# Optimization experiments

Hardware: AMD Instinct MI355X
Metric: run time of the kernel (lower is better)

Reference implementation:

```python
import jax, jax.numpy as jnp
import numpy as np

B, C, S, F = 128, 5, 512, 3
U = 256          # encoder units
RU = 2 * U       # decoder units / bidirectional encoder width


def _lstm_cell(x_t, h, c, Wk, Wr, b):
    # Keras LSTM gate order: i, f, g(cell), o
    z = x_t @ Wk + h @ Wr + b
    i, f, g, o = jnp.split(z, 4, axis=-1)
    c_new = jax.nn.sigmoid(f) * c + jax.nn.sigmoid(i) * jnp.tanh(g)
    h_new = jax.nn.sigmoid(o) * jnp.tanh(c_new)
    return h_new, c_new


def _masked_lstm(xs, mask, Wk, Wr, b, units):
    # xs: [B,S,D], mask: [B,S] bool. Keras semantics: masked steps carry
    # previous state and previous output (== previous h for LSTM).
    Bn = xs.shape[0]

    def step(carry, inp):
        h, c = carry
        x_t, m_t = inp
        h_n, c_n = _lstm_cell(x_t, h, c, Wk, Wr, b)
        m = m_t[:, None]
        h2 = jnp.where(m, h_n, h)
        c2 = jnp.where(m, c_n, c)
        return (h2, c2), h2

    init = (jnp.zeros((Bn, units), xs.dtype), jnp.zeros((Bn, units), xs.dtype))
    _, outs = jax.lax.scan(step, init, (jnp.swapaxes(xs, 0, 1), mask.T))
    return jnp.swapaxes(outs, 0, 1)  # [B,S,units]


def setup_inputs() -> dict:
    key = jax.random.key(0)
    k = jax.random.split(key, 10)
    s = 0.05
    rn = lambda kk, sh: jax.random.normal(kk, sh, jnp.float32) * s
    return {
        "x": jax.random.normal(k[0], (B, C, S, F), jnp.float32),
        "Wf_k": rn(k[1], (C, 4 * U)), "Wf_r": rn(k[2], (U, 4 * U)), "bf": jnp.zeros((4 * U,), jnp.float32),
        "Wb_k": rn(k[3], (C, 4 * U)), "Wb_r": rn(k[4], (U, 4 * U)), "bb": jnp.zeros((4 * U,), jnp.float32),
        "Wd_k": rn(k[5], (C, 4 * RU)), "Wd_r": rn(k[6], (RU, 4 * RU)), "bd": jnp.zeros((4 * RU,), jnp.float32),
        "W_attn": rn(k[7], (RU + C, 1)), "b_attn": jnp.zeros((1,), jnp.float32),
        "W_dense": rn(k[8], (RU + RU, C)), "b_dense": jnp.zeros((C,), jnp.float32),
    }


def reference(x, Wf_k, Wf_r, bf, Wb_k, Wb_r, bb, Wd_k, Wd_r, bd,
              W_attn, b_attn, W_dense, b_dense):
    xt = jnp.transpose(x, (0, 2, 1, 3))          # [B,S,C,F]
    mask = xt[:, :, 0, 2] != 0                   # tf.cast(..., bool)
    xs = xt[:, :, :, 0]                          # [B,S,C]

    fwd = _masked_lstm(xs, mask, Wf_k, Wf_r, bf, U)
    bwd = _masked_lstm(xs[:, ::-1], mask[:, ::-1], Wb_k, Wb_r, bb, U)[:, ::-1]
    enc = jnp.concatenate([fwd, bwd], axis=-1)   # [B,S,RU]

    # attention(concat([tile(x_t), enc])) is linear -> split the weight:
    Wx, We = W_attn[:C, 0], W_attn[C:, 0]
    enc_scores = jnp.einsum('bsd,d->bs', enc, We) + b_attn[0]  # [B,S]

    hidden0 = enc[:, -1, :]                      # [B,RU]
    x0 = xs[:, 0, :]                             # [B,C]

    def dec_step(carry, _):
        hidden, x_t = carry
        scores = enc_scores + (x_t @ Wx)[:, None]             # [B,S]
        alpha = jax.nn.softmax(scores, axis=1)
        attn = jnp.einsum('bs,bsd->bd', alpha, enc)           # [B,RU]
        # decoder LSTM on a single timestep, initial_state=[hidden, attn]
        h_new, _c = _lstm_cell(x_t, hidden, attn, Wd_k, Wd_r, bd)
        x_new = jnp.concatenate([h_new, attn], axis=-1) @ W_dense + b_dense
        return (h_new, x_new), x_new

    _, ys = jax.lax.scan(dec_step, (hidden0, x0), None, length=S - 1)  # [S-1,B,C]
    return jnp.transpose(ys, (1, 2, 0))[..., None]           # [B,C,S-1,1]
```

## Files before the change

### kernel.cpp

```cpp
#include <hip/hip_runtime.h>
#include <math.h>

#define BATCH 128
#define CCH 5
#define SEQ 512
#define UNITS 256
#define RU 512

#define ENC_N 33554432

typedef float v2f __attribute__((ext_vector_type(2)));

__device__ __forceinline__ float sigmoidf_(float v) {
    return 1.0f / (1.0f + __expf(-v));
}
__device__ __forceinline__ float tanhf_(float v) {
    float e = __expf(2.0f * v);
    return 1.0f - 2.0f / (e + 1.0f);
}
__device__ __forceinline__ void astoref(float* p, float v) {
    __hip_atomic_store(p, v, __ATOMIC_RELAXED, __HIP_MEMORY_SCOPE_AGENT);
}
__device__ __forceinline__ void astorei(int* p, int v) {
    __hip_atomic_store(p, v, __ATOMIC_RELAXED, __HIP_MEMORY_SCOPE_AGENT);
}
__device__ __forceinline__ unsigned long long aloadu64(const unsigned long long* p) {
    return __hip_atomic_load(p, __ATOMIC_RELAXED, __HIP_MEMORY_SCOPE_AGENT);
}
__device__ __forceinline__ int aloadi(const int* p) {
    return __hip_atomic_load(p, __ATOMIC_RELAXED, __HIP_MEMORY_SCOPE_AGENT);
}

#define PK_LO(ACC, H2, W2) \
    asm("v_pk_fma_f32 %0, %1, %2, %0 op_sel:[0,0,0] op_sel_hi:[1,0,1]" \
        : "+v"(ACC) : "v"(H2), "v"(W2))
#define PK_HI(ACC, H2, W2) \
    asm("v_pk_fma_f32 %0, %1, %2, %0 op_sel:[0,1,0] op_sel_hi:[1,1,1]" \
        : "+v"(ACC) : "v"(H2), "v"(W2))

__global__ __attribute__((amdgpu_flat_work_group_size(1024, 1024),
                          amdgpu_waves_per_eu(4, 4)))
void encoder_kernel(const float* __restrict__ x,
                    const float* __restrict__ Wf_k, const float* __restrict__ Wf_r,
                    const float* __restrict__ bf,
                    const float* __restrict__ Wb_k, const float* __restrict__ Wb_r,
                    const float* __restrict__ bb,
                    float* __restrict__ enc, float* __restrict__ h_ex,
                    int* __restrict__ flags)
{
    const int bid  = blockIdx.x;
    const int dir  = bid >> 7;
    const int tile = (bid >> 3) & 15;
    const int jsl  = bid & 7;
    const int grp  = dir * 16 + tile;
    const int bg0  = tile * 8;
    const float* __restrict__ Wk   = dir ? Wb_k : Wf_k;
    const float* __restrict__ Wr   = dir ? Wb_r : Wf_r;
    const float* __restrict__ bias = dir ? bb : bf;
    const int tid  = threadIdx.x;
    const int wv   = tid >> 6;
    const int lane = tid & 63;
    const int g0 = ((lane >> 5) << 8) + jsl * 32 + (lane & 31);

    __shared__ float zp[16][8][128];
    __shared__ float __align__(16) hPe[2][4][520];
    __shared__ float WkL[5][128];
    __shared__ float biasL[128];
    __shared__ unsigned char mL[8][SEQ];
    __shared__ float xLe[8][8];

    for (int i = tid; i < 2 * 4 * 520; i += 1024) ((float*)hPe)[i] = 0.0f;
    if (tid < 128) biasL[tid] = bias[((tid >> 5) << 8) + jsl * 32 + (tid & 31)];
    if (tid >= 128 && tid < 768) {
        int i = tid - 128, c = i >> 7, cl = i & 127;
        WkL[c][cl] = Wk[c * 1024 + ((cl >> 5) << 8) + jsl * 32 + (cl & 31)];
    }
    for (int i = tid; i < 8 * SEQ; i += 1024) {
        int b = i >> 9, tt = i & (SEQ - 1);
        mL[b][tt] = (x[((size_t)((bg0 + b) * CCH) * SEQ + tt) * 3 + 2] != 0.0f) ? 1 : 0;
    }
    v2f wp[16];
    {
        const float* wbase = Wr + (size_t)(wv * 16) * 1024 + g0;
        #pragma unroll
        for (int r = 0; r < 16; ++r) {
            v2f w; w.x = wbase[(size_t)r * 1024]; w.y = wbase[(size_t)r * 1024 + 512];
            wp[r] = w;
        }
    }
    float creg = 0.0f;
    __syncthreads();

    for (int t = 0; t < SEQ; ++t) {
        const int cur = t & 1;
        const int ts = dir ? (SEQ - 1 - t) : t;
        if (t > 0) {
            const int* fp = &flags[(grp * 8 + (wv >> 1)) * 32];
            if (lane == 0) {
                int guard = 0;
                while (aloadi(fp) < t && guard < (1 << 26)) {
                    __builtin_amdgcn_s_sleep(1); ++guard;
                }
            }
            int p = lane >> 4, u = wv * 16 + (lane & 15);
            const unsigned long long* hsrc = (const unsigned long long*)
                &h_ex[(size_t)(dir * 2 + ((t - 1) & 1)) * (BATCH * UNITS)];
            unsigned long long v = aloadu64(hsrc + (size_t)((bg0 >> 1) + p) * UNITS + u);
            *(unsigned long long*)&hPe[cur][p][u * 2] = v;
        }
        if (tid >= 960 && tid < 1000) {
            int i = tid - 960, b = i / 5, c = i - b * 5;
            xLe[b][c] = x[((size_t)((bg0 + b) * CCH + c) * SEQ + ts) * 3];
        }
        __syncthreads();

        v2f acc0[4], acc1[4];
        #pragma unroll
        for (int p = 0; p < 4; ++p) { acc0[p] = (v2f){0.f, 0.f}; acc1[p] = (v2f){0.f, 0.f}; }
        #pragma unroll
        for (int q = 0; q < 8; ++q) {
            v2f h[4][2];
            #pragma unroll
            for (int p = 0; p < 4; ++p) {
                float4 A = *(const float4*)&hPe[cur][p][(wv * 16 + q * 2) * 2];
                v2f h0; h0.x = A.x; h0.y = A.y;
                v2f h1; h1.x = A.z; h1.y = A.w;
                h[p][0] = h0; h[p][1] = h1;
            }
            #pragma unroll
            for (int r = 0; r < 2; ++r) {
                v2f w2 = wp[q * 2 + r];
                #pragma unroll
                for (int p = 0; p < 4; ++p) {
                    PK_LO(acc0[p], h[p][r], w2);
                    PK_HI(acc1[p], h[p][r], w2);
                }
            }
        }
        #pragma unroll
        for (int p = 0; p < 4; ++p) {
            zp[wv][2 * p][lane]          = acc0[p].x;
            zp[wv][2 * p + 1][lane]      = acc0[p].y;
            zp[wv][2 * p][64 + lane]     = acc1[p].x;
            zp[wv][2 * p + 1][64 + lane] = acc1[p].y;
        }
        __syncthreads();

        if (tid < 256) {
            int b = tid >> 5, u = tid & 31;
            float zi = biasL[u], zf = biasL[32 + u], zg = biasL[64 + u], zo = biasL[96 + u];
            #pragma unroll
            for (int s = 0; s < 16; ++s) {
                zi += zp[s][b][u];       zf += zp[s][b][32 + u];
                zg += zp[s][b][64 + u];  zo += zp[s][b][96 + u];
            }
            #pragma unroll
            for (int c = 0; c < 5; ++c) {
                float xv = xLe[b][c];
                zi = fmaf(xv, WkL[c][u], zi);      zf = fmaf(xv, WkL[c][32 + u], zf);
                zg = fmaf(xv, WkL[c][64 + u], zg); zo = fmaf(xv, WkL[c][96 + u], zo);
            }
            float cn = sigmoidf_(zf) * creg + sigmoidf_(zi) * tanhf_(zg);
            float hn = sigmoidf_(zo) * tanhf_(cn);
            float hprev = hPe[cur][b >> 1][(jsl * 32 + u) * 2 + (b & 1)];
            float h2 = mL[b][ts] ? hn : hprev;
            float c2 = mL[b][ts] ? cn : creg;
            creg = c2;
            astoref(&h_ex[(size_t)(dir * 2 + cur) * (BATCH * UNITS)
                          + ((size_t)((bg0 + b) >> 1) * UNITS + jsl * 32 + u) * 2 + (b & 1)], h2);
            enc[((size_t)(bg0 + b) * SEQ + ts) * RU + dir * UNITS + jsl * 32 + u] = h2;
        }
        __syncthreads();
        if (tid == 0) astorei(&flags[(grp * 8 + jsl) * 32], t + 1);
    }
}

__global__ __launch_bounds__(256)
void attn_kernel(const float* __restrict__ enc,
                 const float* __restrict__ W_attn, const float* __restrict__ b_attn,
                 const float* __restrict__ W_dense, const float* __restrict__ b_dense,
                 const float* __restrict__ x,
                 float* __restrict__ attn_ws, float* __restrict__ hidden_ws,
                 float* __restrict__ xbuf, float* __restrict__ xconst)
{
    const int b = blockIdx.x;
    const int tid = threadIdx.x;
    const int lane = tid & 63;
    const int wv = tid >> 6;

    __shared__ float WeL[RU];
    __shared__ float scoresL[SEQ];
    __shared__ float red[256];
    __shared__ float attnL[RU];

    WeL[tid]       = W_attn[CCH + tid];
    WeL[tid + 256] = W_attn[CCH + tid + 256];
    __syncthreads();

    const float* __restrict__ encb = enc + (size_t)b * SEQ * RU;
    const float batt = b_attn[0];

    for (int s = wv; s < SEQ; s += 4) {
        const float* row = encb + (size_t)s * RU;
        float p = 0.0f;
        #pragma unroll
        for (int i = 0; i < 8; ++i) {
            int d = lane * 8 + i;
            p = fmaf(row[d], WeL[d], p);
        }
        #pragma unroll
        for (int o = 32; o; o >>= 1) p += __shfl_xor(p, o);
        if (lane == 0) scoresL[s] = p + batt;
    }
    __syncthreads();

    float m = fmaxf(scoresL[tid], scoresL[tid + 256]);
    red[tid] = m;
    __syncthreads();
    for (int st = 128; st; st >>= 1) {
        if (tid < st) red[tid] = fmaxf(red[tid], red[tid + st]);
        __syncthreads();
    }
    const float mx = red[0];
    __syncthreads();
    float e0 = __expf(scoresL[tid] - mx);
    float e1 = __expf(scoresL[tid + 256] - mx);
    red[tid] = e0 + e1;
    __syncthreads();
    for (int st = 128; st; st >>= 1) {
        if (tid < st) red[tid] += red[tid + st];
        __syncthreads();
    }
    const float sinv = 1.0f / red[0];
    __syncthreads();
    scoresL[tid]       = e0 * sinv;
    scoresL[tid + 256] = e1 * sinv;
    __syncthreads();

    float a0 = 0.0f, a1 = 0.0f;
    for (int s = 0; s < SEQ; ++s) {
        float al = scoresL[s];
        a0 = fmaf(al, encb[(size_t)s * RU + tid], a0);
        a1 = fmaf(al, encb[(size_t)s * RU + tid + 256], a1);
    }
    attn_ws[(size_t)b * RU + tid]       = a0;
    attn_ws[(size_t)b * RU + tid + 256] = a1;
    attnL[tid] = a0;
    attnL[tid + 256] = a1;
    hidden_ws[(size_t)b * RU + tid]       = encb[(size_t)(SEQ - 1) * RU + tid];
    hidden_ws[(size_t)b * RU + tid + 256] = encb[(size_t)(SEQ - 1) * RU + tid + 256];
    if (tid < CCH) xbuf[b * CCH + tid] = x[((size_t)(b * CCH + tid) * SEQ + 0) * 3];
    __syncthreads();

    if (tid < CCH) {
        float acc = b_dense[tid];
        for (int d = 0; d < RU; ++d)
            acc = fmaf(attnL[d], W_dense[(RU + d) * CCH + tid], acc);
        xconst[b * CCH + tid] = acc;
    }
}

__global__ __attribute__((amdgpu_flat_work_group_size(1024, 1024),
                          amdgpu_waves_per_eu(4, 4)))
void decoder_kernel(const float* __restrict__ Wd_k, const float* __restrict__ Wd_r,
                    const float* __restrict__ bd,
                    const float* __restrict__ W_dense,
                    const float* __restrict__ attn_ws, const float* __restrict__ hidden_ws,
                    const float* __restrict__ xbuf, const float* __restrict__ xconst,
                    float* __restrict__ h_ex, int* __restrict__ flags,
                    float* __restrict__ out)
{
    const int bid  = blockIdx.x;
    const int tile = bid >> 4;
    const int jsl  = bid & 15;
    const int bg0  = tile * 8;
    const int tid  = threadIdx.x;
    const int wv   = tid >> 6;
    const int lane = tid & 63;
    const int g0 = ((lane >> 5) << 9) + jsl * 32 + (lane & 31);

    __shared__ float zp[16][8][128];
    __shared__ float __align__(16) hPd[2][4][1040];
    __shared__ float WdL[RU * CCH];
    __shared__ float WkL[5][128];
    __shared__ float biasL[128];
    __shared__ float attL[8][32];
    __shared__ float xL[8][8], xcL[8][8];

    for (int i = tid; i < RU * CCH; i += 1024) WdL[i] = W_dense[i];
    if (tid < 128) biasL[tid] = bd[((tid >> 5) << 9) + jsl * 32 + (tid & 31)];
    if (tid >= 128 && tid < 768) {
        int i = tid - 128, c = i >> 7, cl = i & 127;
        WkL[c][cl] = Wd_k[c * 2048 + ((cl >> 5) << 9) + jsl * 32 + (cl & 31)];
    }
    if (tid < 256) {
        int b = tid >> 5, u = tid & 31;
        attL[b][u] = attn_ws[(size_t)(bg0 + b) * RU + jsl * 32 + u];
    }
    if (tid < 64) {
        int b = tid >> 3, c = tid & 7;
        if (c < 5) {
            xL[b][c]  = xbuf[(bg0 + b) * CCH + c];
            xcL[b][c] = xconst[(bg0 + b) * CCH + c];
        }
    }
    for (int e = tid; e < 2048; e += 1024) {
        int p = e >> 9, u = e & 511;
        hPd[0][p][u * 2]     = hidden_ws[(size_t)(bg0 + 2 * p) * RU + u];
        hPd[0][p][u * 2 + 1] = hidden_ws[(size_t)(bg0 + 2 * p + 1) * RU + u];
    }
    v2f wp[32];
    {
        const float* wbase = Wd_r + (size_t)(wv * 32) * 2048 + g0;
        #pragma unroll
        for (int r = 0; r < 32; ++r) {
            v2f w; w.x = wbase[(size_t)r * 2048]; w.y = wbase[(size_t)r * 2048 + 1024];
            wp[r] = w;
        }
    }
    __syncthreads();

    for (int t = 0; t < SEQ - 1; ++t) {
        const int cur = t & 1;
        if (t > 0) {
            const int* fp = &flags[(tile * 16 + wv) * 32];
            if (lane == 0) {
                int guard = 0;
                while (aloadi(fp) < t && guard < (1 << 26)) {
                    __builtin_amdgcn_s_sleep(1); ++guard;
                }
            }
            int p = lane >> 4, u0 = wv * 32 + (lane & 15) * 2;
            const unsigned long long* hsrc = (const unsigned long long*)
                &h_ex[(size_t)((t - 1) & 1) * (BATCH * RU)];
            unsigned long long v0 = aloadu64(hsrc + (size_t)((bg0 >> 1) + p) * RU + u0);
            unsigned long long v1 = aloadu64(hsrc + (size_t)((bg0 >> 1) + p) * RU + u0 + 1);
            *(unsigned long long*)&hPd[cur][p][u0 * 2]       = v0;
            *(unsigned long long*)&hPd[cur][p][(u0 + 1) * 2] = v1;
        }
        __syncthreads();

        if (t > 0) {
            for (int it = wv; it < 40; it += 16) {
                int bb = it / 5, c = it - bb * 5;
                const float* hb = &hPd[cur][bb >> 1][bb & 1];
                float p = 0.f;
                #pragma unroll
                for (int q = 0; q < 8; ++q) {
                    int uu = lane + (q << 6);
                    p = fmaf(hb[uu * 2], WdL[uu * CCH + c], p);
                }
                #pragma unroll
                for (int o = 32; o; o >>= 1) p += __shfl_xor(p, o);
                if (lane == 0) xL[bb][c] = p + xcL[bb][c];
            }
        }

        v2f acc0[4], acc1[4];
        #pragma unroll
        for (int p = 0; p < 4; ++p) { acc0[p] = (v2f){0.f, 0.f}; acc1[p] = (v2f){0.f, 0.f}; }
        #pragma unroll
        for (int q = 0; q < 16; ++q) {
            v2f h[4][2];
            #pragma unroll
            for (int p = 0; p < 4; ++p) {
                float4 A = *(const float4*)&hPd[cur][p][(wv * 32 + q * 2) * 2];
                v2f h0; h0.x = A.x; h0.y = A.y;
                v2f h1; h1.x = A.z; h1.y = A.w;
                h[p][0] = h0; h[p][1] = h1;
            }
            #pragma unroll
            for (int r = 0; r < 2; ++r) {
                v2f w2 = wp[q * 2 + r];
                #pragma unroll
                for (int p = 0; p < 4; ++p) {
                    PK_LO(acc0[p], h[p][r], w2);
                    PK_HI(acc1[p], h[p][r], w2);
                }
            }
        }
        #pragma unroll
        for (int p = 0; p < 4; ++p) {
            zp[wv][2 * p][lane]          = acc0[p].x;
            zp[wv][2 * p + 1][lane]      = acc0[p].y;
            zp[wv][2 * p][64 + lane]     = acc1[p].x;
            zp[wv][2 * p + 1][64 + lane] = acc1[p].y;
        }
        __syncthreads();

        if (tid < 256) {
            int b = tid >> 5, u = tid & 31;
            float zi = biasL[u], zf = biasL[32 + u], zg = biasL[64 + u], zo = biasL[96 + u];
            #pragma unroll
            for (int s = 0; s < 16; ++s) {
                zi += zp[s][b][u];       zf += zp[s][b][32 + u];
                zg += zp[s][b][64 + u];  zo += zp[s][b][96 + u];
            }
            #pragma unroll
            for (int c = 0; c < 5; ++c) {
                float xv = xL[b][c];
                zi = fmaf(xv, WkL[c][u], zi);      zf = fmaf(xv, WkL[c][32 + u], zf);
                zg = fmaf(xv, WkL[c][64 + u], zg); zo = fmaf(xv, WkL[c][96 + u], zo);
            }
            float cn = sigmoidf_(zf) * attL[b][u] + sigmoidf_(zi) * tanhf_(zg);
            float hn = sigmoidf_(zo) * tanhf_(cn);
            astoref(&h_ex[(size_t)cur * (BATCH * RU)
                          + ((size_t)((bg0 + b) >> 1) * RU + jsl * 32 + u) * 2 + (b & 1)], hn);
        }
        __syncthreads();
        if (tid == 0) astorei(&flags[(tile * 16 + jsl) * 32], t + 1);
        if (t > 0 && jsl == 0 && tid >= 256 && tid < 296) {
            int i = tid - 256, bb = i / 5, c = i - bb * 5;
            out[(size_t)((bg0 + bb) * CCH + c) * (SEQ - 1) + (t - 1)] = xL[bb][c];
        }
    }

    {
        const int t = SEQ - 1;
        const int cur = t & 1;
        const int* fp = &flags[(tile * 16 + wv) * 32];
        if (lane == 0) {
            int guard = 0;
            while (aloadi(fp) < t && guard < (1 << 26)) {
                __builtin_amdgcn_s_sleep(1); ++guard;
            }
        }
        int p = lane >> 4, u0 = wv * 32 + (lane & 15) * 2;
        const unsigned long long* hsrc = (const unsigned long long*)
            &h_ex[(size_t)((t - 1) & 1) * (BATCH * RU)];
        unsigned long long v0 = aloadu64(hsrc + (size_t)((bg0 >> 1) + p) * RU + u0);
        unsigned long long v1 = aloadu64(hsrc + (size_t)((bg0 >> 1) + p) * RU + u0 + 1);
        *(unsigned long long*)&hPd[cur][p][u0 * 2]       = v0;
        *(unsigned long long*)&hPd[cur][p][(u0 + 1) * 2] = v1;
        __syncthreads();
        if (jsl == 0) {
            for (int it = wv; it < 40; it += 16) {
                int bb = it / 5, c = it - bb * 5;
                const float* hb = &hPd[cur][bb >> 1][bb & 1];
                float p2 = 0.f;
                #pragma unroll
                for (int q = 0; q < 8; ++q) {
                    int uu = lane + (q << 6);
                    p2 = fmaf(hb[uu * 2], WdL[uu * CCH + c], p2);
                }
                #pragma unroll
                for (int o = 32; o; o >>= 1) p2 += __shfl_xor(p2, o);
                if (lane == 0)
                    out[(size_t)((bg0 + bb) * CCH + c) * (SEQ - 1) + (t - 1)]
                        = p2 + xcL[bb][c];
            }
        }
    }
}

extern "C" void kernel_launch(void* const* d_in, const int* in_sizes, int n_in,
                              void* d_out, int out_size, void* d_ws, size_t ws_size,
                              hipStream_t stream)
{
    const float* x       = (const float*)d_in[0];
    const float* Wf_k    = (const float*)d_in[1];
    const float* Wf_r    = (const float*)d_in[2];
    const float* bf      = (const float*)d_in[3];
    const float* Wb_k    = (const float*)d_in[4];
    const float* Wb_r    = (const float*)d_in[5];
    const float* bb      = (const float*)d_in[6];
    const float* Wd_k    = (const float*)d_in[7];
    const float* Wd_r    = (const float*)d_in[8];
    const float* bd      = (const float*)d_in[9];
    const float* W_attn  = (const float*)d_in[10];
    const float* b_attn  = (const float*)d_in[11];
    const float* W_dense = (const float*)d_in[12];
    const float* b_dense = (const float*)d_in[13];
    float* out = (float*)d_out;

    float* ws = (float*)d_ws;
    float* enc      = ws;
    float* attn_p   = ws + ENC_N;
    float* hidden_p = ws + ENC_N + 65536;
    float* xbuf_p   = ws + ENC_N + 131072;
    float* xconst_p = ws + ENC_N + 131712;
    float* h_ex_e   = ws + ENC_N;
    int*   flag_e   = (int*)(ws + ENC_N + 131072);
    int*   flag_d   = (int*)ws;
    float* h_ex_d   = ws + 8192;

    hipMemsetAsync(flag_e, 0, 8192 * sizeof(int), stream);
    encoder_kernel<<<256, 1024, 0, stream>>>(x, Wf_k, Wf_r, bf, Wb_k, Wb_r, bb,
                                             enc, h_ex_e, flag_e);
    attn_kernel<<<BATCH, 256, 0, stream>>>(enc, W_attn, b_attn, W_dense, b_dense, x,
                                           attn_p, hidden_p, xbuf_p, xconst_p);
    hipMemsetAsync(flag_d, 0, 8192 * sizeof(int), stream);
    decoder_kernel<<<256, 1024, 0, stream>>>(Wd_k, Wd_r, bd, W_dense,
                                             attn_p, hidden_p, xbuf_p, xconst_p,
                                             h_ex_d, flag_d, out);
}
```

Baseline: 5.599 ms.

## Replace LDS partial-sum reduction with in-register shuffle butterfly in LSTM kernels

Both recurrent kernels now split the K dimension across 32 lanes per unit. Each lane accumulates all four gates for all eight batches, and the partials are reduced with a wave-level shuffle butterfly instead of being written to a shared zp buffer and summed by 256 threads after an extra barrier. The hidden-state exchange layout is changed to unit-major with padded LDS addressing, and bias, input weights and cell state move into per-lane registers. This removes a block barrier and the LDS reduction pass per step, at the cost of many cross-lane shuffles and a reworked, riskier exchange layout.

Result: slower. 7.775 ms (+38.9%).

```diff
diff --git a/kernel.cpp b/kernel.cpp
--- a/kernel.cpp
+++ b/kernel.cpp
@@ -37,6 +37,56 @@
 #define PK_HI(ACC, H2, W2) \
     asm("v_pk_fma_f32 %0, %1, %2, %0 op_sel:[0,1,0] op_sel_hi:[1,1,1]" \
         : "+v"(ACC) : "v"(H2), "v"(W2))
+
+#define HADDR_D(u, b) ((u) * 8 + ((u) >> 4) * 2 + (b))
+#define HADDR_E(u, b) ((u) * 8 + ((u) >> 3) * 2 + (b))
+
+#define BUTTERFLY(ACC, L, ZRES) { \
+    v2f m1_[2][4]; \
+    const bool k4_ = ((L) & 16); \
+    _Pragma("unroll") \
+    for (int p2_ = 0; p2_ < 2; ++p2_) { \
+        _Pragma("unroll") \
+        for (int j_ = 0; j_ < 4; ++j_) { \
+            v2f lo_ = ACC[p2_][j_], hi_ = ACC[2 + p2_][j_]; \
+            float olx = __shfl(lo_.x, (L) ^ 16), oly = __shfl(lo_.y, (L) ^ 16); \
+            float ohx = __shfl(hi_.x, (L) ^ 16), ohy = __shfl(hi_.y, (L) ^ 16); \
+            m1_[p2_][j_].x = k4_ ? (hi_.x + ohx) : (lo_.x + olx); \
+            m1_[p2_][j_].y = k4_ ? (hi_.y + ohy) : (lo_.y + oly); \
+        } \
+    } \
+    v2f m2_[4]; \
+    const bool k3_ = ((L) & 8); \
+    _Pragma("unroll") \
+    for (int j_ = 0; j_ < 4; ++j_) { \
+        v2f lo_ = m1_[0][j_], hi_ = m1_[1][j_]; \
+        float olx = __shfl(lo_.x, (L) ^ 8), oly = __shfl(lo_.y, (L) ^ 8); \
+        float ohx = __shfl(hi_.x, (L) ^ 8), ohy = __shfl(hi_.y, (L) ^ 8); \
+        m2_[j_].x = k3_ ? (hi_.x + ohx) : (lo_.x + olx); \
+        m2_[j_].y = k3_ ? (hi_.y + ohy) : (lo_.y + oly); \
+    } \
+    float m3_[4]; \
+    const bool k2_ = ((L) & 4); \
+    _Pragma("unroll") \
+    for (int j_ = 0; j_ < 4; ++j_) { \
+        float xo_ = __shfl(m2_[j_].x, (L) ^ 4); \
+        float yo_ = __shfl(m2_[j_].y, (L) ^ 4); \
+        m3_[j_] = k2_ ? (m2_[j_].y + yo_) : (m2_[j_].x + xo_); \
+    } \
+    float m4_[2]; \
+    const bool k1_ = ((L) & 2); \
+    _Pragma("unroll") \
+    for (int jj_ = 0; jj_ < 2; ++jj_) { \
+        float a_ = m3_[jj_], b_ = m3_[2 + jj_]; \
+        float ao_ = __shfl(a_, (L) ^ 2), bo_ = __shfl(b_, (L) ^ 2); \
+        m4_[jj_] = k1_ ? (b_ + bo_) : (a_ + ao_); \
+    } \
+    { \
+        float a_ = m4_[0], b_ = m4_[1]; \
+        float ao_ = __shfl(a_, (L) ^ 1), bo_ = __shfl(b_, (L) ^ 1); \
+        ZRES = ((L) & 1) ? (b_ + bo_) : (a_ + ao_); \
+    } \
+}
 
 __global__ __attribute__((amdgpu_flat_work_group_size(1024, 1024),
                           amdgpu_waves_per_eu(4, 4)))
@@ -57,38 +107,39 @@
     const float* __restrict__ Wk   = dir ? Wb_k : Wf_k;
     const float* __restrict__ Wr   = dir ? Wb_r : Wf_r;
     const float* __restrict__ bias = dir ? bb : bf;
-    const int tid  = threadIdx.x;
-    const int wv   = tid >> 6;
-    const int lane = tid & 63;
-    const int g0 = ((lane >> 5) << 8) + jsl * 32 + (lane & 31);
-
-    __shared__ float zp[16][8][128];
-    __shared__ float __align__(16) hPe[2][4][520];
-    __shared__ float WkL[5][128];
-    __shared__ float biasL[128];
+    const int tid = threadIdx.x;
+    const int wv  = tid >> 6;
+    const int l   = tid & 63;
+    const int s   = l & 31;
+    const int u_idx = wv * 2 + (l >> 5);
+    const int U     = jsl * 32 + u_idx;
+    const int b_ln  = s >> 2;
+    const int g_ln  = s & 3;
+
+    __shared__ float hTe[2][2112];
     __shared__ unsigned char mL[8][SEQ];
     __shared__ float xLe[8][8];
 
-    for (int i = tid; i < 2 * 4 * 520; i += 1024) ((float*)hPe)[i] = 0.0f;
-    if (tid < 128) biasL[tid] = bias[((tid >> 5) << 8) + jsl * 32 + (tid & 31)];
-    if (tid >= 128 && tid < 768) {
-        int i = tid - 128, c = i >> 7, cl = i & 127;
-        WkL[c][cl] = Wk[c * 1024 + ((cl >> 5) << 8) + jsl * 32 + (cl & 31)];
-    }
+    for (int i = tid; i < 2 * 2112; i += 1024) ((float*)hTe)[i] = 0.0f;
     for (int i = tid; i < 8 * SEQ; i += 1024) {
         int b = i >> 9, tt = i & (SEQ - 1);
         mL[b][tt] = (x[((size_t)((bg0 + b) * CCH) * SEQ + tt) * 3 + 2] != 0.0f) ? 1 : 0;
     }
-    v2f wp[16];
+    v2f w01[8], w23[8];
     {
-        const float* wbase = Wr + (size_t)(wv * 16) * 1024 + g0;
-        #pragma unroll
-        for (int r = 0; r < 16; ++r) {
-            v2f w; w.x = wbase[(size_t)r * 1024]; w.y = wbase[(size_t)r * 1024 + 512];
-            wp[r] = w;
-        }
-    }
-    float creg = 0.0f;
+        const float* wb = Wr + (size_t)(s * 8) * 1024 + U;
+        #pragma unroll
+        for (int r = 0; r < 8; ++r) {
+            v2f a; a.x = wb[(size_t)r * 1024];        a.y = wb[(size_t)r * 1024 + 256];
+            v2f c; c.x = wb[(size_t)r * 1024 + 512];  c.y = wb[(size_t)r * 1024 + 768];
+            w01[r] = a; w23[r] = c;
+        }
+    }
+    const float biasR = bias[g_ln * 256 + U];
+    float wkR[CCH];
+    #pragma unroll
+    for (int c = 0; c < CCH; ++c) wkR[c] = Wk[c * 1024 + g_ln * 256 + U];
+    float creg = 0.0f, hreg = 0.0f;
     __syncthreads();
 
     for (int t = 0; t < SEQ; ++t) {
@@ -96,17 +147,18 @@
         const int ts = dir ? (SEQ - 1 - t) : t;
         if (t > 0) {
             const int* fp = &flags[(grp * 8 + (wv >> 1)) * 32];
-            if (lane == 0) {
+            if (l == 0) {
                 int guard = 0;
                 while (aloadi(fp) < t && guard < (1 << 26)) {
                     __builtin_amdgcn_s_sleep(1); ++guard;
                 }
             }
-            int p = lane >> 4, u = wv * 16 + (lane & 15);
+            int u = wv * 16 + (l >> 2), b0 = (l & 3) * 2;
             const unsigned long long* hsrc = (const unsigned long long*)
-                &h_ex[(size_t)(dir * 2 + ((t - 1) & 1)) * (BATCH * UNITS)];
-            unsigned long long v = aloadu64(hsrc + (size_t)((bg0 >> 1) + p) * UNITS + u);
-            *(unsigned long long*)&hPe[cur][p][u * 2] = v;
+                &h_ex[(size_t)(dir * 2 + ((t - 1) & 1)) * 32768 + tile * 2048
+                      + (size_t)u * 8 + b0];
+            unsigned long long v = aloadu64(hsrc);
+            *(unsigned long long*)&hTe[cur][HADDR_E(u, b0)] = v;
         }
         if (tid >= 960 && tid < 1000) {
             int i = tid - 960, b = i / 5, c = i - b * 5;
@@ -114,61 +166,47 @@
         }
         __syncthreads();
 
-        v2f acc0[4], acc1[4];
-        #pragma unroll
-        for (int p = 0; p < 4; ++p) { acc0[p] = (v2f){0.f, 0.f}; acc1[p] = (v2f){0.f, 0.f}; }
-        #pragma unroll
-        for (int q = 0; q < 8; ++q) {
-            v2f h[4][2];
+        v2f acc[4][4];
+        #pragma unroll
+        for (int p = 0; p < 4; ++p)
+            #pragma unroll
+            for (int j = 0; j < 4; ++j) acc[p][j] = (v2f){0.f, 0.f};
+        const float* hrow = &hTe[cur][s * 66];
+        #pragma unroll
+        for (int rr = 0; rr < 8; ++rr) {
+            const v2f* hp = (const v2f*)(hrow + rr * 8);
+            v2f a = w01[rr], c = w23[rr];
             #pragma unroll
             for (int p = 0; p < 4; ++p) {
-                float4 A = *(const float4*)&hPe[cur][p][(wv * 16 + q * 2) * 2];
-                v2f h0; h0.x = A.x; h0.y = A.y;
-                v2f h1; h1.x = A.z; h1.y = A.w;
-                h[p][0] = h0; h[p][1] = h1;
-            }
-            #pragma unroll
-            for (int r = 0; r < 2; ++r) {
-                v2f w2 = wp[q * 2 + r];
-                #pragma unroll
-                for (int p = 0; p < 4; ++p) {
-                    PK_LO(acc0[p], h[p][r], w2);
-                    PK_HI(acc1[p], h[p][r], w2);
-                }
-            }
-        }
-        #pragma unroll
-        for (int p = 0; p < 4; ++p) {
-            zp[wv][2 * p][lane]          = acc0[p].x;
-            zp[wv][2 * p + 1][lane]      = acc0[p].y;
-            zp[wv][2 * p][64 + lane]     = acc1[p].x;
-            zp[wv][2 * p + 1][64 + lane] = acc1[p].y;
-        }
-        __syncthreads();
-
-        if (tid < 256) {
-            int b = tid >> 5, u = tid & 31;
-            float zi = biasL[u], zf = biasL[32 + u], zg = biasL[64 + u], zo = biasL[96 + u];
-            #pragma unroll
-            for (int s = 0; s < 16; ++s) {
-                zi += zp[s][b][u];       zf += zp[s][b][32 + u];
-                zg += zp[s][b][64 + u];  zo += zp[s][b][96 + u];
-            }
-            #pragma unroll
-            for (int c = 0; c < 5; ++c) {
-                float xv = xLe[b][c];
-                zi = fmaf(xv, WkL[c][u], zi);      zf = fmaf(xv, WkL[c][32 + u], zf);
-                zg = fmaf(xv, WkL[c][64 + u], zg); zo = fmaf(xv, WkL[c][96 + u], zo);
-            }
-            float cn = sigmoidf_(zf) * creg + sigmoidf_(zi) * tanhf_(zg);
-            float hn = sigmoidf_(zo) * tanhf_(cn);
-            float hprev = hPe[cur][b >> 1][(jsl * 32 + u) * 2 + (b & 1)];
-            float h2 = mL[b][ts] ? hn : hprev;
-            float c2 = mL[b][ts] ? cn : creg;
-            creg = c2;
-            astoref(&h_ex[(size_t)(dir * 2 + cur) * (BATCH * UNITS)
-                          + ((size_t)((bg0 + b) >> 1) * UNITS + jsl * 32 + u) * 2 + (b & 1)], h2);
-            enc[((size_t)(bg0 + b) * SEQ + ts) * RU + dir * UNITS + jsl * 32 + u] = h2;
+                v2f h2 = hp[p];
+                PK_LO(acc[p][0], h2, a);
+                PK_HI(acc[p][1], h2, a);
+                PK_LO(acc[p][2], h2, c);
+                PK_HI(acc[p][3], h2, c);
+            }
+        }
+
+        float z;
+        BUTTERFLY(acc, l, z)
+        z += biasR;
+        #pragma unroll
+        for (int c = 0; c < CCH; ++c) z = fmaf(xLe[b_ln][c], wkR[c], z);
+        float T = (g_ln == 2) ? tanhf_(z) : sigmoidf_(z);
+        const int base = l & ~3;
+        float Ti = __shfl(T, base);
+        float Tf = __shfl(T, base + 1);
+        float Tg = __shfl(T, base + 2);
+        float To = __shfl(T, base + 3);
+        float cn = Tf * creg + Ti * Tg;
+        float hn = To * tanhf_(cn);
+        int m = mL[b_ln][ts];
+        float h2v = m ? hn : hreg;
+        float c2v = m ? cn : creg;
+        creg = c2v; hreg = h2v;
+        if ((l & 3) == 0) {
+            astoref(&h_ex[(size_t)(dir * 2 + cur) * 32768 + tile * 2048
+                          + (size_t)U * 8 + b_ln], h2v);
+            enc[((size_t)(bg0 + b_ln) * SEQ + ts) * RU + dir * UNITS + U] = h2v;
         }
         __syncthreads();
         if (tid == 0) astorei(&flags[(grp * 8 + jsl) * 32], t + 1);
@@ -276,27 +314,18 @@
     const int bg0  = tile * 8;
     const int tid  = threadIdx.x;
     const int wv   = tid >> 6;
-    const int lane = tid & 63;
-    const int g0 = ((lane >> 5) << 9) + jsl * 32 + (lane & 31);
-
-    __shared__ float zp[16][8][128];
-    __shared__ float __align__(16) hPd[2][4][1040];
+    const int l    = tid & 63;
+    const int s    = l & 31;
+    const int u_idx = wv * 2 + (l >> 5);
+    const int U     = jsl * 32 + u_idx;
+    const int b_ln  = s >> 2;
+    const int g_ln  = s & 3;
+
+    __shared__ float hT[2][4160];
     __shared__ float WdL[RU * CCH];
-    __shared__ float WkL[5][128];
-    __shared__ float biasL[128];
-    __shared__ float attL[8][32];
     __shared__ float xL[8][8], xcL[8][8];
 
     for (int i = tid; i < RU * CCH; i += 1024) WdL[i] = W_dense[i];
-    if (tid < 128) biasL[tid] = bd[((tid >> 5) << 9) + jsl * 32 + (tid & 31)];
-    if (tid >= 128 && tid < 768) {
-        int i = tid - 128, c = i >> 7, cl = i & 127;
-        WkL[c][cl] = Wd_k[c * 2048 + ((cl >> 5) << 9) + jsl * 32 + (cl & 31)];
-    }
-    if (tid < 256) {
-        int b = tid >> 5, u = tid & 31;
-        attL[b][u] = attn_ws[(size_t)(bg0 + b) * RU + jsl * 32 + u];
-    }
     if (tid < 64) {
         int b = tid >> 3, c = tid & 7;
         if (c < 5) {
@@ -304,109 +333,100 @@
             xcL[b][c] = xconst[(bg0 + b) * CCH + c];
         }
     }
-    for (int e = tid; e < 2048; e += 1024) {
-        int p = e >> 9, u = e & 511;
-        hPd[0][p][u * 2]     = hidden_ws[(size_t)(bg0 + 2 * p) * RU + u];
-        hPd[0][p][u * 2 + 1] = hidden_ws[(size_t)(bg0 + 2 * p + 1) * RU + u];
-    }
-    v2f wp[32];
+    for (int e = tid; e < 4096; e += 1024) {
+        int u = e >> 3, b = e & 7;
+        hT[0][HADDR_D(u, b)] = hidden_ws[(size_t)(bg0 + b) * RU + u];
+    }
+    v2f w01[16], w23[16];
     {
-        const float* wbase = Wd_r + (size_t)(wv * 32) * 2048 + g0;
-        #pragma unroll
-        for (int r = 0; r < 32; ++r) {
-            v2f w; w.x = wbase[(size_t)r * 2048]; w.y = wbase[(size_t)r * 2048 + 1024];
-            wp[r] = w;
-        }
-    }
+        const float* wb = Wd_r + (size_t)(s * 16) * 2048 + U;
+        #pragma unroll
+        for (int r = 0; r < 16; ++r) {
+            v2f a; a.x = wb[(size_t)r * 2048];         a.y = wb[(size_t)r * 2048 + 512];
+            v2f c; c.x = wb[(size_t)r * 2048 + 1024];  c.y = wb[(size_t)r * 2048 + 1536];
+            w01[r] = a; w23[r] = c;
+        }
+    }
+    const float biasR = bd[g_ln * 512 + U];
+    float wkR[CCH];
+    #pragma unroll
+    for (int c = 0; c < CCH; ++c) wkR[c] = Wd_k[c * 2048 + g_ln * 512 + U];
+    const float attR = attn_ws[(size_t)(bg0 + b_ln) * RU + U];
     __syncthreads();
 
     for (int t = 0; t < SEQ - 1; ++t) {
         const int cur = t & 1;
         if (t > 0) {
             const int* fp = &flags[(tile * 16 + wv) * 32];
-            if (lane == 0) {
+            if (l == 0) {
                 int guard = 0;
                 while (aloadi(fp) < t && guard < (1 << 26)) {
                     __builtin_amdgcn_s_sleep(1); ++guard;
                 }
             }
-            int p = lane >> 4, u0 = wv * 32 + (lane & 15) * 2;
+            int u = wv * 32 + (l >> 1), b0 = (l & 1) * 4;
             const unsigned long long* hsrc = (const unsigned long long*)
-                &h_ex[(size_t)((t - 1) & 1) * (BATCH * RU)];
-            unsigned long long v0 = aloadu64(hsrc + (size_t)((bg0 >> 1) + p) * RU + u0);
-            unsigned long long v1 = aloadu64(hsrc + (size_t)((bg0 >> 1) + p) * RU + u0 + 1);
-            *(unsigned long long*)&hPd[cur][p][u0 * 2]       = v0;
-            *(unsigned long long*)&hPd[cur][p][(u0 + 1) * 2] = v1;
+                &h_ex[(size_t)((t - 1) & 1) * 65536 + tile * 4096
+                      + (size_t)u * 8 + b0];
+            unsigned long long v0 = aloadu64(hsrc);
+            unsigned long long v1 = aloadu64(hsrc + 1);
+            *(unsigned long long*)&hT[cur][HADDR_D(u, b0)]     = v0;
+            *(unsigned long long*)&hT[cur][HADDR_D(u, b0 + 2)] = v1;
         }
         __syncthreads();
 
         if (t > 0) {
             for (int it = wv; it < 40; it += 16) {
                 int bb = it / 5, c = it - bb * 5;
-                const float* hb = &hPd[cur][bb >> 1][bb & 1];
                 float p = 0.f;
                 #pragma unroll
                 for (int q = 0; q < 8; ++q) {
-                    int uu = lane + (q << 6);
-                    p = fmaf(hb[uu * 2], WdL[uu * CCH + c], p);
+                    int uu = l + (q << 6);
+                    p = fmaf(hT[cur][HADDR_D(uu, bb)], WdL[uu * CCH + c], p);
                 }
                 #pragma unroll
                 for (int o = 32; o; o >>= 1) p += __shfl_xor(p, o);
-                if (lane == 0) xL[bb][c] = p + xcL[bb][c];
-            }
-        }
-
-        v2f acc0[4], acc1[4];
-        #pragma unroll
-        for (int p = 0; p < 4; ++p) { acc0[p] = (v2f){0.f, 0.f}; acc1[p] = (v2f){0.f, 0.f}; }
-        #pragma unroll
-        for (int q = 0; q < 16; ++q) {
-            v2f h[4][2];
+                if (l == 0) xL[bb][c] = p + xcL[bb][c];
+            }
+        }
+
+        v2f acc[4][4];
+        #pragma unroll
+        for (int p = 0; p < 4; ++p)
+            #pragma unroll
+            for (int j = 0; j < 4; ++j) acc[p][j] = (v2f){0.f, 0.f};
+        const float* hrow = &hT[cur][s * 130];
+        #pragma unroll
+        for (int rr = 0; rr < 16; ++rr) {
+            const v2f* hp = (const v2f*)(hrow + rr * 8);
+            v2f a = w01[rr], c = w23[rr];
             #pragma unroll
             for (int p = 0; p < 4; ++p) {
-                float4 A = *(const float4*)&hPd[cur][p][(wv * 32 + q * 2) * 2];
-                v2f h0; h0.x = A.x; h0.y = A.y;
-                v2f h1; h1.x = A.z; h1.y = A.w;
-                h[p][0] = h0; h[p][1] = h1;
-            }
-            #pragma unroll
-            for (int r = 0; r < 2; ++r) {
-                v2f w2 = wp[q * 2 + r];
-                #pragma unroll
-                for (int p = 0; p < 4; ++p) {
-                    PK_LO(acc0[p], h[p][r], w2);
-                    PK_HI(acc1[p], h[p][r], w2);
-                }
-            }
-        }
-        #pragma unroll
-        for (int p = 0; p < 4; ++p) {
-            zp[wv][2 * p][lane]          = acc0[p].x;
-            zp[wv][2 * p + 1][lane]      = acc0[p].y;
-            zp[wv][2 * p][64 + lane]     = acc1[p].x;
-            zp[wv][2 * p + 1][64 + lane] = acc1[p].y;
-        }
-        __syncthreads();
-
-        if (tid < 256) {
-            int b = tid >> 5, u = tid & 31;
-            float zi = biasL[u], zf = biasL[32 + u], zg = biasL[64 + u], zo = biasL[96 + u];
-            #pragma unroll
-            for (int s = 0; s < 16; ++s) {
-                zi += zp[s][b][u];       zf += zp[s][b][32 + u];
-                zg += zp[s][b][64 + u];  zo += zp[s][b][96 + u];
-            }
-            #pragma unroll
-            for (int c = 0; c < 5; ++c) {
-                float xv = xL[b][c];
-                zi = fmaf(xv, WkL[c][u], zi);      zf = fmaf(xv, WkL[c][32 + u], zf);
-                zg = fmaf(xv, WkL[c][64 + u], zg); zo = fmaf(xv, WkL[c][96 + u], zo);
-            }
-            float cn = sigmoidf_(zf) * attL[b][u] + sigmoidf_(zi) * tanhf_(zg);
-            float hn = sigmoidf_(zo) * tanhf_(cn);
-            astoref(&h_ex[(size_t)cur * (BATCH * RU)
-                          + ((size_t)((bg0 + b) >> 1) * RU + jsl * 32 + u) * 2 + (b & 1)], hn);
-        }
+                v2f h2 = hp[p];
+                PK_LO(acc[p][0], h2, a);
+                PK_HI(acc[p][1], h2, a);
+                PK_LO(acc[p][2], h2, c);
+                PK_HI(acc[p][3], h2, c);
+            }
+        }
+        __syncthreads();
+
+        float z;
+        BUTTERFLY(acc, l, z)
+        z += biasR;
+        #pragma unroll
+        for (int c = 0; c < CCH; ++c) z = fmaf(xL[b_ln][c], wkR[c], z);
+        float T = (g_ln == 2) ? tanhf_(z) : sigmoidf_(z);
+        const int base = l & ~3;
+        float Ti = __shfl(T, base);
+        float Tf = __shfl(T, base + 1);
+        float Tg = __shfl(T, base + 2);
+        float To = __shfl(T, base + 3);
+        float cn = Tf * attR + Ti * Tg;
+        float hn = To * tanhf_(cn);
+        if ((l & 3) == 0)
+            astoref(&h_ex[(size_t)cur * 65536 + tile * 4096
+                          + (size_t)U * 8 + b_ln], hn);
         __syncthreads();
         if (tid == 0) astorei(&flags[(tile * 16 + jsl) * 32], t + 1);
         if (t > 0 && jsl == 0 && tid >= 256 && tid < 296) {
@@ -415,40 +435,38 @@
         }
     }
 
-    {
+    if (jsl == 0) {
         const int t = SEQ - 1;
         const int cur = t & 1;
         const int* fp = &flags[(tile * 16 + wv) * 32];
-        if (lane == 0) {
+        if (l == 0) {
             int guard = 0;
             while (aloadi(fp) < t && guard < (1 << 26)) {
                 __builtin_amdgcn_s_sleep(1); ++guard;
             }
         }
-        int p = lane >> 4, u0 = wv * 32 + (lane & 15) * 2;
+        int u = wv * 32 + (l >> 1), b0 = (l & 1) * 4;
         const unsigned long long* hsrc = (const unsigned long long*)
-            &h_ex[(size_t)((t - 1) & 1) * (BATCH * RU)];
-        unsigned long long v0 = aloadu64(hsrc + (size_t)((bg0 >> 1) + p) * RU + u0);
-        unsigned long long v1 = aloadu64(hsrc + (size_t)((bg0 >> 1) + p) * RU + u0 + 1);
-        *(unsigned long long*)&hPd[cur][p][u0 * 2]       = v0;
-        *(unsigned long long*)&hPd[cur][p][(u0 + 1) * 2] = v1;
-        __syncthreads();
-        if (jsl == 0) {
-            for (int it = wv; it < 40; it += 16) {
-                int bb = it / 5, c = it - bb * 5;
-                const float* hb = &hPd[cur][bb >> 1][bb & 1];
-                float p2 = 0.f;
-                #pragma unroll
-                for (int q = 0; q < 8; ++q) {
-                    int uu = lane + (q << 6);
-                    p2 = fmaf(hb[uu * 2], WdL[uu * CCH + c], p2);
-                }
-                #pragma unroll
-                for (int o = 32; o; o >>= 1) p2 += __shfl_xor(p2, o);
-                if (lane == 0)
-                    out[(size_t)((bg0 + bb) * CCH + c) * (SEQ - 1) + (t - 1)]
-                        = p2 + xcL[bb][c];
-            }
+            &h_ex[(size_t)((t - 1) & 1) * 65536 + tile * 4096
+                  + (size_t)u * 8 + b0];
+        unsigned long long v0 = aloadu64(hsrc);
+        unsigned long long v1 = aloadu64(hsrc + 1);
+        *(unsigned long long*)&hT[cur][HADDR_D(u, b0)]     = v0;
+        *(unsigned long long*)&hT[cur][HADDR_D(u, b0 + 2)] = v1;
+        __syncthreads();
+        for (int it = wv; it < 40; it += 16) {
+            int bb = it / 5, c = it - bb * 5;
+            float p = 0.f;
+            #pragma unroll
+            for (int q = 0; q < 8; ++q) {
+                int uu = l + (q << 6);
+                p = fmaf(hT[cur][HADDR_D(uu, bb)], WdL[uu * CCH + c], p);
+            }
+            #pragma unroll
+            for (int o = 32; o; o >>= 1) p += __shfl_xor(p, o);
+            if (l == 0)
+                out[(size_t)((bg0 + bb) * CCH + c) * (SEQ - 1) + (t - 1)]
+                    = p + xcL[bb][c];
         }
     }
 }
```
